# Kernel optimization log

Measured on AMD Instinct MI355X. Metric: run time of the kernel, lower is better.

Reference implementation:

```python
import jax, jax.numpy as jnp
import numpy as np

N = 4096
IN_F = 512
OUT_F = 512


def setup_inputs() -> dict:
    key = jax.random.key(0)
    k1, k2, k3, k4 = jax.random.split(key, 4)
    x = jax.random.normal(k1, (N, IN_F), dtype=jnp.float32)
    adj = jax.random.uniform(k2, (N, N), dtype=jnp.float32)
    # linear params (torch nn.Linear default init: U(-1/sqrt(fan_in), 1/sqrt(fan_in)))
    bound = 1.0 / np.sqrt(IN_F)
    W = jax.random.uniform(k3, (OUT_F, IN_F), minval=-bound, maxval=bound, dtype=jnp.float32)
    b = jax.random.uniform(k4, (OUT_F,), minval=-bound, maxval=bound, dtype=jnp.float32)
    return {"x": x, "adj": adj, "W": W, "b": b}


def reference(x, adj, W, b):
    # adj_hat = adj + I
    adj_hat = adj + jnp.eye(adj.shape[0], dtype=adj.dtype)
    # deg is diagonal with 1/sqrt(rowsum); deg @ adj @ deg == d[:,None] * adj * d[None,:]
    d = 1.0 / jnp.sqrt(adj_hat.sum(axis=1))  # [N]
    norm_adj = d[:, None] * adj_hat * d[None, :]  # [N, N]
    h = norm_adj @ x  # [N, in_features]
    return h @ W.T + b  # [N, out_features]
```

## Files before the change

kernel.cpp:

```cpp
#include <hip/hip_runtime.h>
#include <cstdint>

#define NN 4096
#define FF 512

typedef short bf16x8 __attribute__((ext_vector_type(8)));
typedef float f32x4 __attribute__((ext_vector_type(4)));

__device__ __forceinline__ uint16_t f2bf(float f) {
    uint32_t u = __builtin_bit_cast(uint32_t, f);
    u += 0x7FFFu + ((u >> 16) & 1u);
    return (uint16_t)(u >> 16);
}

__global__ __launch_bounds__(256) void k_prep(const float* __restrict__ adj,
                                              float* __restrict__ d,
                                              uint16_t* __restrict__ Abf) {
    const int row  = blockIdx.x * 4 + (threadIdx.x >> 6);
    const int lane = threadIdx.x & 63;
    const float4* p = (const float4*)(adj + (size_t)row * NN);
    float4 v[16];
    float s = 0.f;
#pragma unroll
    for (int i = 0; i < 16; ++i) {
        v[i] = p[lane + i * 64];
        s += (v[i].x + v[i].y) + (v[i].z + v[i].w);
    }
#pragma unroll
    for (int off = 1; off < 64; off <<= 1) s += __shfl_xor(s, off);
    const float di = rsqrtf(s + 1.0f);
    if (lane == 0) d[row] = di;
    uint16_t* outp = Abf + (size_t)row * NN;
#pragma unroll
    for (int i = 0; i < 16; ++i) {
        const int cb = (lane + i * 64) * 4;
        float a0 = v[i].x, a1 = v[i].y, a2 = v[i].z, a3 = v[i].w;
        if (cb + 0 == row) a0 += 1.0f;
        if (cb + 1 == row) a1 += 1.0f;
        if (cb + 2 == row) a2 += 1.0f;
        if (cb + 3 == row) a3 += 1.0f;
        ushort4 o;
        o.x = f2bf(a0); o.y = f2bf(a1); o.z = f2bf(a2); o.w = f2bf(a3);
        *(ushort4*)(outp + cb) = o;
    }
}

__global__ __launch_bounds__(256) void k_xc(const float* __restrict__ x,
                                            uint16_t* __restrict__ xbf) {
    const size_t t4 = (size_t)blockIdx.x * 256 + threadIdx.x;
    float4 v = *(const float4*)(x + t4 * 4);
    ushort4 o;
    o.x = f2bf(v.x); o.y = f2bf(v.y); o.z = f2bf(v.z); o.w = f2bf(v.w);
    *(ushort4*)(xbf + t4 * 4) = o;
}

__global__ __launch_bounds__(256) void k_wc(const float* __restrict__ W,
                                            uint16_t* __restrict__ Wbf) {
    const size_t t4 = (size_t)blockIdx.x * 256 + threadIdx.x;
    float4 v = *(const float4*)(W + t4 * 4);
    ushort4 o;
    o.x = f2bf(v.x); o.y = f2bf(v.y); o.z = f2bf(v.z); o.w = f2bf(v.w);
    *(ushort4*)(Wbf + t4 * 4) = o;
}

__global__ __launch_bounds__(256) void k_zt(const float* __restrict__ z32,
                                            const float* __restrict__ d,
                                            uint16_t* __restrict__ zdT) {
    __shared__ uint16_t t[64][72];
    const int k0 = blockIdx.x * 64;
    const int n0 = blockIdx.y * 64;
    const int tid = threadIdx.x;
    const int r   = tid >> 4;
    const int c4  = tid & 15;
#pragma unroll
    for (int pass = 0; pass < 4; ++pass) {
        const int row = pass * 16 + r;
        float4 v = *(const float4*)(z32 + (size_t)(k0 + row) * FF + n0 + c4 * 4);
        const float dk = d[k0 + row];
        t[c4 * 4 + 0][row] = f2bf(v.x * dk);
        t[c4 * 4 + 1][row] = f2bf(v.y * dk);
        t[c4 * 4 + 2][row] = f2bf(v.z * dk);
        t[c4 * 4 + 3][row] = f2bf(v.w * dk);
    }
    __syncthreads();
#pragma unroll
    for (int pass = 0; pass < 2; ++pass) {
        const int cid = pass * 256 + tid;
        const int n  = cid >> 3;
        const int ch = cid & 7;
        *(uint4*)(zdT + (size_t)(n0 + n) * NN + k0 + ch * 8) = *(const uint4*)&t[n][ch * 8];
    }
}

template <int BM, int BN, int K, int SPLITK>
__global__ __launch_bounds__(256, 4) void k_mm(const uint16_t* __restrict__ A,
                                               const uint16_t* __restrict__ Bt,
                                               float* __restrict__ outp) {
    constexpr int MT    = NN / BM;
    constexpr int NTC   = FF / BN;
    constexpr int KSLEN = K / SPLITK;
    constexpr int NT    = KSLEN / 64;
    constexpr int MTX   = MT / 8;
    constexpr int MFR   = BM / 32;
    constexpr int NFR   = BN / 32;
    constexpr int LPT_A = BM / 32;
    constexpr int LPT_B = BN / 32;

    __shared__ uint16_t As[BM * 64];
    __shared__ uint16_t Bs[BN * 64];

    const int id   = blockIdx.x;
    const int slot = id >> 3;
    const int mt   = (id & 7) * MTX + slot / (NTC * SPLITK);
    const int rem  = slot % (NTC * SPLITK);
    const int nt   = rem % NTC;
    const int ks   = rem / NTC;
    const int m0 = mt * BM;
    const int n0 = nt * BN;
    const int k0 = ks * KSLEN;

    const int tid  = threadIdx.x;
    const int w    = tid >> 6;
    const int lane = tid & 63;
    const int wm = w >> 1, wn = w & 1;

    f32x4 acc[MFR][NFR] = {};

    for (int t = 0; t < NT; ++t) {
        const int ktb = k0 + t * 64;
#pragma unroll
        for (int i = 0; i < LPT_A; ++i) {
            const int boff = i * 4096 + tid * 16;
            const int row  = boff >> 7;
            const int q    = (boff >> 4) & 7;
            const int c    = q ^ (row & 7);
            const uint16_t* src = A + (size_t)(m0 + row) * K + ktb + c * 8;
            __builtin_amdgcn_global_load_lds(
                (const __attribute__((address_space(1))) void*)src,
                (__attribute__((address_space(3))) void*)&As[boff >> 1],
                16, 0, 0);
        }
#pragma unroll
        for (int i = 0; i < LPT_B; ++i) {
            const int boff = i * 4096 + tid * 16;
            const int row  = boff >> 7;
            const int q    = (boff >> 4) & 7;
            const int c    = q ^ (row & 7);
            const uint16_t* src = Bt + (size_t)(n0 + row) * K + ktb + c * 8;
            __builtin_amdgcn_global_load_lds(
                (const __attribute__((address_space(1))) void*)src,
                (__attribute__((address_space(3))) void*)&Bs[boff >> 1],
                16, 0, 0);
        }
        __syncthreads();

#pragma unroll
        for (int kk = 0; kk < 2; ++kk) {
            const int cl = kk * 4 + (lane >> 4);
            bf16x8 af[MFR], bfr[NFR];
#pragma unroll
            for (int mf = 0; mf < MFR; ++mf) {
                const int r = wm * (MFR * 16) + mf * 16 + (lane & 15);
                af[mf] = *(const bf16x8*)&As[r * 64 + ((cl ^ (r & 7)) << 3)];
            }
#pragma unroll
            for (int nf = 0; nf < NFR; ++nf) {
                const int r = wn * (NFR * 16) + nf * 16 + (lane & 15);
                bfr[nf] = *(const bf16x8*)&Bs[r * 64 + ((cl ^ (r & 7)) << 3)];
            }
#pragma unroll
            for (int mf = 0; mf < MFR; ++mf)
#pragma unroll
                for (int nf = 0; nf < NFR; ++nf)
                    acc[mf][nf] = __builtin_amdgcn_mfma_f32_16x16x32_bf16(
                        af[mf], bfr[nf], acc[mf][nf], 0, 0, 0);
        }
        __syncthreads();
    }

    float* dst = outp + (size_t)ks * NN * FF;
    const int rbase = m0 + wm * (MFR * 16) + ((lane >> 4) << 2);
    const int cbase = n0 + wn * (NFR * 16) + (lane & 15);
#pragma unroll
    for (int mf = 0; mf < MFR; ++mf) {
#pragma unroll
        for (int nf = 0; nf < NFR; ++nf) {
            const int col = cbase + nf * 16;
#pragma unroll
            for (int r = 0; r < 4; ++r) {
                const int row = rbase + mf * 16 + r;
                dst[(size_t)row * FF + col] = acc[mf][nf][r];
            }
        }
    }
}

__global__ __launch_bounds__(256) void k_red(const float* __restrict__ parts,
                                             const float* __restrict__ d,
                                             const float* __restrict__ b,
                                             float* __restrict__ out) {
    constexpr size_t STRIDE = (size_t)NN * FF;
    const size_t g   = (size_t)blockIdx.x * 256 + threadIdx.x;
    const int    row = (int)((g * 4) >> 9);
    const int    col = (int)((g * 4) & 511);
    float4 s = *(const float4*)(parts + g * 4);
#pragma unroll
    for (int p = 1; p < 4; ++p) {
        float4 v = *(const float4*)(parts + p * STRIDE + g * 4);
        s.x += v.x; s.y += v.y; s.z += v.z; s.w += v.w;
    }
    const float di = d[row];
    const float4 bv = *(const float4*)(b + col);
    float4 o;
    o.x = s.x * di + bv.x;
    o.y = s.y * di + bv.y;
    o.z = s.z * di + bv.z;
    o.w = s.w * di + bv.w;
    *(float4*)(out + g * 4) = o;
}

extern "C" void kernel_launch(void* const* d_in, const int* in_sizes, int n_in,
                              void* d_out, int out_size, void* d_ws, size_t ws_size,
                              hipStream_t stream) {
    const float* x   = (const float*)d_in[0];
    const float* adj = (const float*)d_in[1];
    const float* W   = (const float*)d_in[2];
    const float* b   = (const float*)d_in[3];
    float* out = (float*)d_out;

    char* ws = (char*)d_ws;
    float*    d_    = (float*)ws;
    uint16_t* Abf   = (uint16_t*)(ws + 65536);
    uint16_t* zdT   = Abf + (size_t)NN * NN;
    uint16_t* xbf   = zdT + (size_t)FF * NN;
    uint16_t* Wbf   = xbf + (size_t)NN * FF;
    float*    z32   = (float*)(Wbf + (size_t)FF * FF);
    float*    parts = z32 + (size_t)NN * FF;

    k_wc<<<FF * FF / 1024, 256, 0, stream>>>(W, Wbf);
    k_xc<<<NN * FF / 1024, 256, 0, stream>>>(x, xbf);
    k_prep<<<NN / 4, 256, 0, stream>>>(adj, d_, Abf);
    k_mm<64, 64, FF, 1><<<512, 256, 0, stream>>>(xbf, Wbf, z32);
    k_zt<<<dim3(NN / 64, FF / 64), 256, 0, stream>>>(z32, d_, zdT);
    k_mm<128, 64, NN, 4><<<1024, 256, 0, stream>>>(Abf, zdT, parts);
    k_red<<<NN * FF / 1024, 256, 0, stream>>>(parts, d_, b, out);
}
```

Baseline: 71.17 us.

## Add triple-buffered large-tile split-K GEMM with bf16 partials for adjacency product

Replaces the 128x64 split-K GEMM for the big adjacency product with a dedicated 256x128-tile, 512-thread kernel that triple-buffers LDS loads using explicit vmcnt waits, so global loads overlap MFMA compute. Block-to-XCD mapping is changed so each XCD pair handles one K split, which is meant to improve L2 locality. Partial sums are stored as bf16 instead of fp32, halving reduction traffic, and the reduce kernel processes 8 elements per thread. Risks include lower occupancy (one 512-thread block per CU, large LDS), only 256 blocks, and precision loss from bf16 partials.

```diff
diff --git a/kernel.cpp b/kernel.cpp
--- a/kernel.cpp
+++ b/kernel.cpp
@@ -11,6 +11,10 @@
     uint32_t u = __builtin_bit_cast(uint32_t, f);
     u += 0x7FFFu + ((u >> 16) & 1u);
     return (uint16_t)(u >> 16);
+}
+__device__ __forceinline__ float bf2f(uint16_t h) {
+    uint32_t u = (uint32_t)h << 16;
+    return __builtin_bit_cast(float, u);
 }
 
 __global__ __launch_bounds__(256) void k_prep(const float* __restrict__ adj,
@@ -92,15 +96,12 @@
     }
 }
 
-template <int BM, int BN, int K, int SPLITK>
+template <int BM, int BN, int K>
 __global__ __launch_bounds__(256, 4) void k_mm(const uint16_t* __restrict__ A,
                                                const uint16_t* __restrict__ Bt,
                                                float* __restrict__ outp) {
-    constexpr int MT    = NN / BM;
     constexpr int NTC   = FF / BN;
-    constexpr int KSLEN = K / SPLITK;
-    constexpr int NT    = KSLEN / 64;
-    constexpr int MTX   = MT / 8;
+    constexpr int NT    = K / 64;
     constexpr int MFR   = BM / 32;
     constexpr int NFR   = BN / 32;
     constexpr int LPT_A = BM / 32;
@@ -110,14 +111,10 @@
     __shared__ uint16_t Bs[BN * 64];
 
     const int id   = blockIdx.x;
-    const int slot = id >> 3;
-    const int mt   = (id & 7) * MTX + slot / (NTC * SPLITK);
-    const int rem  = slot % (NTC * SPLITK);
-    const int nt   = rem % NTC;
-    const int ks   = rem / NTC;
+    const int mt   = id / NTC;
+    const int nt   = id % NTC;
     const int m0 = mt * BM;
     const int n0 = nt * BN;
-    const int k0 = ks * KSLEN;
 
     const int tid  = threadIdx.x;
     const int w    = tid >> 6;
@@ -127,7 +124,7 @@
     f32x4 acc[MFR][NFR] = {};
 
     for (int t = 0; t < NT; ++t) {
-        const int ktb = k0 + t * 64;
+        const int ktb = t * 64;
 #pragma unroll
         for (int i = 0; i < LPT_A; ++i) {
             const int boff = i * 4096 + tid * 16;
@@ -153,7 +150,6 @@
                 16, 0, 0);
         }
         __syncthreads();
-
 #pragma unroll
         for (int kk = 0; kk < 2; ++kk) {
             const int cl = kk * 4 + (lane >> 4);
@@ -178,45 +174,163 @@
         __syncthreads();
     }
 
-    float* dst = outp + (size_t)ks * NN * FF;
     const int rbase = m0 + wm * (MFR * 16) + ((lane >> 4) << 2);
     const int cbase = n0 + wn * (NFR * 16) + (lane & 15);
 #pragma unroll
-    for (int mf = 0; mf < MFR; ++mf) {
+    for (int mf = 0; mf < MFR; ++mf)
 #pragma unroll
         for (int nf = 0; nf < NFR; ++nf) {
             const int col = cbase + nf * 16;
 #pragma unroll
             for (int r = 0; r < 4; ++r) {
                 const int row = rbase + mf * 16 + r;
-                dst[(size_t)row * FF + col] = acc[mf][nf][r];
-            }
-        }
-    }
-}
-
-__global__ __launch_bounds__(256) void k_red(const float* __restrict__ parts,
+                outp[(size_t)row * FF + col] = acc[mf][nf][r];
+            }
+        }
+}
+
+__global__ __launch_bounds__(512, 1) void k_mmx(const uint16_t* __restrict__ A,
+                                                const uint16_t* __restrict__ Bt,
+                                                uint16_t* __restrict__ parts) {
+    constexpr int BM = 256, BN = 128, K = NN;
+    constexpr int KSLEN = K / 4;
+    constexpr int NT    = KSLEN / 64;
+
+    __shared__ uint16_t As[3][BM * 64];
+    __shared__ uint16_t Bs[3][BN * 64];
+
+    const int id   = blockIdx.x;
+    const int xcd  = id & 7;
+    const int slot = id >> 3;
+    const int ks   = xcd >> 1;
+    const int mt   = ((slot >> 2) << 1) | (xcd & 1);
+    const int nt   = slot & 3;
+    const int m0 = mt * BM;
+    const int n0 = nt * BN;
+    const int k0 = ks * KSLEN;
+
+    const int tid  = threadIdx.x;
+    const int w    = tid >> 6;
+    const int lane = tid & 63;
+    const int wm = w >> 1, wn = w & 1;
+
+    f32x4 acc[4][4] = {};
+
+    auto STAGE = [&](int t, int buf) {
+        const int ktb = k0 + t * 64;
+#pragma unroll
+        for (int i = 0; i < 4; ++i) {
+            const int boff = i * 8192 + tid * 16;
+            const int row  = boff >> 7;
+            const int q    = (boff >> 4) & 7;
+            const int c    = q ^ (row & 7);
+            const uint16_t* src = A + (size_t)(m0 + row) * K + ktb + c * 8;
+            __builtin_amdgcn_global_load_lds(
+                (const __attribute__((address_space(1))) void*)src,
+                (__attribute__((address_space(3))) void*)&As[buf][boff >> 1],
+                16, 0, 0);
+        }
+#pragma unroll
+        for (int i = 0; i < 2; ++i) {
+            const int boff = i * 8192 + tid * 16;
+            const int row  = boff >> 7;
+            const int q    = (boff >> 4) & 7;
+            const int c    = q ^ (row & 7);
+            const uint16_t* src = Bt + (size_t)(n0 + row) * K + ktb + c * 8;
+            __builtin_amdgcn_global_load_lds(
+                (const __attribute__((address_space(1))) void*)src,
+                (__attribute__((address_space(3))) void*)&Bs[buf][boff >> 1],
+                16, 0, 0);
+        }
+    };
+
+    auto COMPUTE = [&](int buf) {
+#pragma unroll
+        for (int kk = 0; kk < 2; ++kk) {
+            const int cl = kk * 4 + (lane >> 4);
+            bf16x8 af[4], bfr[4];
+#pragma unroll
+            for (int mf = 0; mf < 4; ++mf) {
+                const int r = wm * 64 + mf * 16 + (lane & 15);
+                af[mf] = *(const bf16x8*)&As[buf][r * 64 + ((cl ^ (r & 7)) << 3)];
+            }
+#pragma unroll
+            for (int nf = 0; nf < 4; ++nf) {
+                const int r = wn * 64 + nf * 16 + (lane & 15);
+                bfr[nf] = *(const bf16x8*)&Bs[buf][r * 64 + ((cl ^ (r & 7)) << 3)];
+            }
+#pragma unroll
+            for (int mf = 0; mf < 4; ++mf)
+#pragma unroll
+                for (int nf = 0; nf < 4; ++nf)
+                    acc[mf][nf] = __builtin_amdgcn_mfma_f32_16x16x32_bf16(
+                        af[mf], bfr[nf], acc[mf][nf], 0, 0, 0);
+        }
+    };
+
+    STAGE(0, 0);
+    STAGE(1, 1);
+    int sb = 2, cb = 0;
+    for (int t = 0; t < NT; ++t) {
+        if (t + 2 < NT) {
+            STAGE(t + 2, sb);
+            sb = (sb == 2) ? 0 : sb + 1;
+            asm volatile("s_waitcnt vmcnt(12)" ::: "memory");
+        } else if (t + 2 == NT) {
+            asm volatile("s_waitcnt vmcnt(6)" ::: "memory");
+        } else {
+            asm volatile("s_waitcnt vmcnt(0)" ::: "memory");
+        }
+        __builtin_amdgcn_s_barrier();
+        COMPUTE(cb);
+        cb = (cb == 2) ? 0 : cb + 1;
+        __builtin_amdgcn_s_barrier();
+    }
+
+    uint16_t* dst = parts + (size_t)ks * NN * FF;
+    const int rbase = m0 + wm * 64 + ((lane >> 4) << 2);
+    const int cbase = n0 + wn * 64 + (lane & 15);
+#pragma unroll
+    for (int mf = 0; mf < 4; ++mf)
+#pragma unroll
+        for (int nf = 0; nf < 4; ++nf) {
+            const int col = cbase + nf * 16;
+#pragma unroll
+            for (int r = 0; r < 4; ++r) {
+                const int row = rbase + mf * 16 + r;
+                dst[(size_t)row * FF + col] = f2bf(acc[mf][nf][r]);
+            }
+        }
+}
+
+__global__ __launch_bounds__(256) void k_red(const uint16_t* __restrict__ parts,
                                              const float* __restrict__ d,
                                              const float* __restrict__ b,
                                              float* __restrict__ out) {
     constexpr size_t STRIDE = (size_t)NN * FF;
     const size_t g   = (size_t)blockIdx.x * 256 + threadIdx.x;
-    const int    row = (int)((g * 4) >> 9);
-    const int    col = (int)((g * 4) & 511);
-    float4 s = *(const float4*)(parts + g * 4);
-#pragma unroll
-    for (int p = 1; p < 4; ++p) {
-        float4 v = *(const float4*)(parts + p * STRIDE + g * 4);
-        s.x += v.x; s.y += v.y; s.z += v.z; s.w += v.w;
+    const int    row = (int)((g * 8) >> 9);
+    const int    col = (int)((g * 8) & 511);
+    float s[8] = {};
+#pragma unroll
+    for (int p = 0; p < 4; ++p) {
+        ushort4 v0 = *(const ushort4*)(parts + p * STRIDE + g * 8);
+        ushort4 v1 = *(const ushort4*)(parts + p * STRIDE + g * 8 + 4);
+        s[0] += bf2f(v0.x); s[1] += bf2f(v0.y); s[2] += bf2f(v0.z); s[3] += bf2f(v0.w);
+        s[4] += bf2f(v1.x); s[5] += bf2f(v1.y); s[6] += bf2f(v1.z); s[7] += bf2f(v1.w);
     }
     const float di = d[row];
-    const float4 bv = *(const float4*)(b + col);
-    float4 o;
-    o.x = s.x * di + bv.x;
-    o.y = s.y * di + bv.y;
-    o.z = s.z * di + bv.z;
-    o.w = s.w * di + bv.w;
-    *(float4*)(out + g * 4) = o;
+    float4 o0, o1;
+    o0.x = s[0] * di + b[col + 0];
+    o0.y = s[1] * di + b[col + 1];
+    o0.z = s[2] * di + b[col + 2];
+    o0.w = s[3] * di + b[col + 3];
+    o1.x = s[4] * di + b[col + 4];
+    o1.y = s[5] * di + b[col + 5];
+    o1.z = s[6] * di + b[col + 6];
+    o1.w = s[7] * di + b[col + 7];
+    *(float4*)(out + g * 8)     = o0;
+    *(float4*)(out + g * 8 + 4) = o1;
 }
 
 extern "C" void kernel_launch(void* const* d_in, const int* in_sizes, int n_in,
@@ -235,13 +349,13 @@
     uint16_t* xbf   = zdT + (size_t)FF * NN;
     uint16_t* Wbf   = xbf + (size_t)NN * FF;
     float*    z32   = (float*)(Wbf + (size_t)FF * FF);
-    float*    parts = z32 + (size_t)NN * FF;
+    uint16_t* parts = (uint16_t*)(z32 + (size_t)NN * FF);
 
     k_wc<<<FF * FF / 1024, 256, 0, stream>>>(W, Wbf);
     k_xc<<<NN * FF / 1024, 256, 0, stream>>>(x, xbf);
     k_prep<<<NN / 4, 256, 0, stream>>>(adj, d_, Abf);
-    k_mm<64, 64, FF, 1><<<512, 256, 0, stream>>>(xbf, Wbf, z32);
+    k_mm<64, 64, FF><<<512, 256, 0, stream>>>(xbf, Wbf, z32);
     k_zt<<<dim3(NN / 64, FF / 64), 256, 0, stream>>>(z32, d_, zdT);
-    k_mm<128, 64, NN, 4><<<1024, 256, 0, stream>>>(Abf, zdT, parts);
-    k_red<<<NN * FF / 1024, 256, 0, stream>>>(parts, d_, b, out);
-}
+    k_mmx<<<256, 512, 0, stream>>>(Abf, zdT, parts);
+    k_red<<<NN * FF / 2048, 256, 0, stream>>>(parts, d_, b, out);
+}
```

New measurement: 68.87 us. -3.2%, faster.
